# Performance work log

Measured on AMD Instinct MI355X. Metric: run time of the kernel, lower is better.

The kernel has to match this reference:

```python
import jax, jax.numpy as jnp
import numpy as np
from jax import lax

B, T, F, D, K = 64, 1000, 140, 256, 7
TAU, V_TH, EPS, ALPHA = 2.0, 1.0, 1e-5, 2.0
PAD = (K - 1) // 2

# Heaviside spike with ATan surrogate gradient (spikingjelly default, alpha=2)
@jax.custom_vjp
def spike_fn(x):
    return (x >= 0.0).astype(x.dtype)

def _spike_fwd(x):
    return spike_fn(x), x

def _spike_bwd(x, g):
    sg = (ALPHA / 2.0) / (1.0 + (jnp.pi / 2.0 * ALPHA * x) ** 2)
    return (g * sg,)

spike_fn.defvjp(_spike_fwd, _spike_bwd)

def lif(x_seq):
    """Multi-step LIF: v += (x - v)/tau, hard reset to 0 on spike. x_seq: (T,B,D)."""
    def step(v, x):
        v = v + (x - v) / TAU
        s = spike_fn(v - V_TH)
        return v * (1.0 - s), s
    _, spikes = lax.scan(step, jnp.zeros_like(x_seq[0]), x_seq)
    return spikes

def bn(x, g, b, m, v):
    # eval-mode BatchNorm1d over channel dim D (last axis of (T,B,D))
    return (x - m) * (g * lax.rsqrt(v + EPS)) + b

def setup_inputs() -> dict:
    key = jax.random.key(0)
    ks = jax.random.split(key, 4)
    s = 0.05
    return {
        "x": jax.random.normal(ks[0], (B, T, F), jnp.float32),
        "pw_w": jax.random.normal(ks[1], (D, F), jnp.float32) * s,
        "pw_b": jnp.zeros((D,), jnp.float32),
        "dw_w": jax.random.normal(ks[2], (D, 1, K), jnp.float32) * s,  # depthwise (O,I/g,K)
        "bn1_g": jnp.ones((D,), jnp.float32),
        "bn1_b": jnp.zeros((D,), jnp.float32),
        "bn1_m": jnp.zeros((D,), jnp.float32),
        "bn1_v": jnp.ones((D,), jnp.float32),
        "lin_w": jax.random.normal(ks[3], (D, D), jnp.float32) * s,
        "bn2_g": jnp.ones((D,), jnp.float32),
        "bn2_b": jnp.zeros((D,), jnp.float32),
        "bn2_m": jnp.zeros((D,), jnp.float32),
        "bn2_v": jnp.ones((D,), jnp.float32),
    }

def reference(x, pw_w, pw_b, dw_w, bn1_g, bn1_b, bn1_m, bn1_v,
              lin_w, bn2_g, bn2_b, bn2_m, bn2_v):
    # pointwise conv: (B,T,F) -> (B,D,T)
    h = jnp.einsum('btf,df->bdt', x, pw_w) + pw_b[None, :, None]
    # depthwise temporal conv, groups=D, same padding
    h = lax.conv_general_dilated(h, dw_w, window_strides=(1,),
                                 padding=[(PAD, PAD)], feature_group_count=D,
                                 dimension_numbers=('NCH', 'OIH', 'NCH'))
    h = jnp.transpose(h, (2, 0, 1))  # (T,B,D) multi-step layout
    h = lif(bn(h, bn1_g, bn1_b, bn1_m, bn1_v))
    residual = h
    h = jnp.einsum('tbd,ed->tbe', h, lin_w)
    h = lif(bn(h, bn2_g, bn2_b, bn2_m, bn2_v))
    return h + residual
```

## Files before the change

kernel.cpp:

```cpp
#include <hip/hip_runtime.h>
#include <hip/hip_bf16.h>

#define B_  64
#define T_  1000
#define F_  140
#define D_  256
#define EPS_ 1e-5f

#define CL_ 50
#define NC_ 20
#define W_  24
#define ROWS_ (CL_ + W_ + 6)

typedef __attribute__((ext_vector_type(8))) short bf16x8;
typedef __attribute__((ext_vector_type(4))) float f32x4;

static __device__ inline short f2bf(float f) {
  __hip_bfloat16 h = __float2bfloat16(f);
  return *reinterpret_cast<short*>(&h);
}
static __device__ inline float bf2f(short s) {
  unsigned int u = ((unsigned int)(unsigned short)s) << 16;
  return __uint_as_float(u);
}

__global__ __launch_bounds__(256) void k0_transpose(const float* __restrict__ lw,
                                                    float* __restrict__ lwT) {
  int i = blockIdx.x * 256 + threadIdx.x;
  int e = i >> 8, d = i & 255;
  lwT[(size_t)d * D_ + e] = lw[(size_t)e * D_ + d];
}

#define KP_ 40
__global__ __launch_bounds__(256) void k1_mfma(const float* __restrict__ x,
                                               const float* __restrict__ w,
                                               const float* __restrict__ bias,
                                               __hip_bfloat16* __restrict__ h) {
  __shared__ short smem[2 * 128 * KP_ * 2];
  short* As = smem;
  short* Bs = smem + 2 * 128 * KP_;
  const int m0 = blockIdx.x * 128;
  const int n0 = blockIdx.y * 128;
  const int tid = threadIdx.x;
  const int lane = tid & 63, wv = tid >> 6;
  const int lr = lane & 15, quad = lane >> 4;
  const int mr = (wv & 1) * 64, nc = (wv >> 1) * 64;

  const int srow = tid >> 1;
  const int sc4 = (tid & 1) * 4;

  auto stage = [&](int kc, int buf) {
#pragma unroll
    for (int c = 0; c < 4; c++) {
      int c4 = sc4 + c;
      int kg = kc + c4 * 4;
      float4 av = make_float4(0.f, 0.f, 0.f, 0.f);
      float4 bv = make_float4(0.f, 0.f, 0.f, 0.f);
      if (kg < F_) {
        av = *(const float4*)(x + (size_t)(m0 + srow) * F_ + kg);
        bv = *(const float4*)(w + (size_t)(n0 + srow) * F_ + kg);
      }
      short* ap = As + buf * 128 * KP_ + srow * KP_ + c4 * 4;
      short* bp = Bs + buf * 128 * KP_ + srow * KP_ + c4 * 4;
      ap[0] = f2bf(av.x); ap[1] = f2bf(av.y); ap[2] = f2bf(av.z); ap[3] = f2bf(av.w);
      bp[0] = f2bf(bv.x); bp[1] = f2bf(bv.y); bp[2] = f2bf(bv.z); bp[3] = f2bf(bv.w);
    }
  };

  f32x4 acc[4][4] = {};
  stage(0, 0);
  __syncthreads();
#pragma unroll
  for (int kk = 0; kk < 5; kk++) {
    const int cur = kk & 1;
    if (kk < 4) stage((kk + 1) * 32, cur ^ 1);
    const short* ab = As + cur * 128 * KP_ + quad * 8;
    const short* bb = Bs + cur * 128 * KP_ + quad * 8;
    bf16x8 a[4], b[4];
#pragma unroll
    for (int i = 0; i < 4; i++) a[i] = *(const bf16x8*)(ab + (mr + i * 16 + lr) * KP_);
#pragma unroll
    for (int j = 0; j < 4; j++) b[j] = *(const bf16x8*)(bb + (nc + j * 16 + lr) * KP_);
#pragma unroll
    for (int i = 0; i < 4; i++)
#pragma unroll
      for (int j = 0; j < 4; j++)
        acc[i][j] = __builtin_amdgcn_mfma_f32_16x16x32_bf16(a[i], b[j], acc[i][j], 0, 0, 0);
    __syncthreads();
  }

  short* Cs = smem;
#pragma unroll
  for (int j = 0; j < 4; j++) {
    const int n = nc + j * 16 + lr;
    const float badd = bias[n0 + n];
#pragma unroll
    for (int i = 0; i < 4; i++) {
      const int mrow = mr + i * 16 + quad * 4;
#pragma unroll
      for (int r = 0; r < 4; r++)
        Cs[(mrow + r) * 136 + n] = f2bf(acc[i][j][r] + badd);
    }
  }
  __syncthreads();
  const int row = tid >> 1, half = tid & 1;
  const int m = m0 + row;
  const int bb2 = m / T_;
  const int t = m - bb2 * T_;
  __hip_bfloat16* dst = h + ((size_t)t * B_ + bb2) * D_ + n0 + half * 64;
  const short* src = Cs + row * 136 + half * 64;
#pragma unroll
  for (int c = 0; c < 4; c++)
    *(int4*)(dst + c * 8) = *(const int4*)(src + c * 8);
}

__global__ __launch_bounds__(256) void k2_dw_lif(const __hip_bfloat16* __restrict__ h,
                                                 const float* __restrict__ dww,
                                                 const float* __restrict__ g1,
                                                 const float* __restrict__ b1,
                                                 const float* __restrict__ m1,
                                                 const float* __restrict__ v1,
                                                 unsigned long long* __restrict__ bits) {
  __shared__ short hs[ROWS_ * D_];
  const int b = blockIdx.x;
  const int t0 = blockIdx.y * CL_;
  const int tstart = (t0 >= W_) ? t0 - W_ : 0;
  const int nwarm = t0 - tstart;
  const int nrows = nwarm + CL_ + 6;
  const int tid = threadIdx.x;

  {
    const int c8 = (tid & 31) * 8;
    for (int r = tid >> 5; r < nrows; r += 8) {
      const int t = tstart - 3 + r;
      bf16x8 val = {0, 0, 0, 0, 0, 0, 0, 0};
      if (t >= 0 && t < T_)
        val = *(const bf16x8*)((const short*)h + ((size_t)t * B_ + b) * D_ + c8);
      *(bf16x8*)(hs + r * D_ + c8) = val;
    }
  }
  __syncthreads();

  const int d = tid;
  float w[7];
#pragma unroll
  for (int k = 0; k < 7; k++) w[k] = dww[d * 7 + k];
  const float sc = g1[d] * rsqrtf(v1[d] + EPS_);
  const float shf = b1[d] - m1[d] * sc;

  float win0 = bf2f(hs[0 * D_ + d]);
  float win1 = bf2f(hs[1 * D_ + d]);
  float win2 = bf2f(hs[2 * D_ + d]);
  float win3 = bf2f(hs[3 * D_ + d]);
  float win4 = bf2f(hs[4 * D_ + d]);
  float win5 = bf2f(hs[5 * D_ + d]);
  float v = 0.f;
  int s = 0;
  for (; s < nwarm; s++) {
    float tap6 = bf2f(hs[(s + 6) * D_ + d]);
    float conv = win0 * w[0] + win1 * w[1] + win2 * w[2] + win3 * w[3] +
                 win4 * w[4] + win5 * w[5] + tap6 * w[6];
    float u = conv * sc + shf;
    v = 0.5f * (v + u);
    v = (v >= 1.0f) ? 0.f : v;
    win0 = win1; win1 = win2; win2 = win3; win3 = win4; win4 = win5; win5 = tap6;
  }
  unsigned long long* bp = bits + ((size_t)b * T_ + t0) * 4 + (tid >> 6);
  const bool lane0 = (tid & 63) == 0;
#pragma unroll 5
  for (int i = 0; i < CL_; i++, s++) {
    float tap6 = bf2f(hs[(s + 6) * D_ + d]);
    float conv = win0 * w[0] + win1 * w[1] + win2 * w[2] + win3 * w[3] +
                 win4 * w[4] + win5 * w[5] + tap6 * w[6];
    float u = conv * sc + shf;
    v = 0.5f * (v + u);
    bool sp = (v >= 1.0f);
    unsigned long long mask = __ballot(sp);
    if (lane0) bp[(size_t)i * 4] = mask;
    v = sp ? 0.f : v;
    win0 = win1; win1 = win2; win2 = win3; win3 = win4; win4 = win5; win5 = tap6;
  }
}

__global__ __launch_bounds__(256) void k3_lin_lif(const unsigned long long* __restrict__ bits,
                                                  const float* __restrict__ lwT,
                                                  const float* __restrict__ g2,
                                                  const float* __restrict__ b2,
                                                  const float* __restrict__ m2,
                                                  const float* __restrict__ v2,
                                                  float* __restrict__ out) {
  __shared__ unsigned long long sb[(CL_ + W_) * 4];
  const int b = blockIdx.x;
  const int t0 = blockIdx.y * CL_;
  const int tstart = (t0 >= W_) ? t0 - W_ : 0;
  const int nwarm = t0 - tstart;
  const int nsteps = nwarm + CL_;
  const int e = threadIdx.x;
  const unsigned long long* gbp = bits + ((size_t)b * T_ + tstart) * 4;
  for (int i = e; i < nsteps * 4; i += 256) sb[i] = gbp[i];
  __syncthreads();

  const float sc = g2[e] * rsqrtf(v2[e] + EPS_);
  const float shf = b2[e] - m2[e] * sc;
  const int eq = e >> 6, eb = e & 63;
  float v = 0.f;
  int s = 0;
  for (; s < nwarm; s++) {
    unsigned long long w0 = sb[s * 4 + 0], w1 = sb[s * 4 + 1];
    unsigned long long w2 = sb[s * 4 + 2], w3 = sb[s * 4 + 3];
    float acc = 0.f;
    if (w0 | w1 | w2 | w3) {
      unsigned long long mm;
      mm = w0; while (mm) { int l = __builtin_ctzll(mm); mm &= mm - 1; acc += lwT[(size_t)(l) * D_ + e]; }
      mm = w1; while (mm) { int l = __builtin_ctzll(mm); mm &= mm - 1; acc += lwT[(size_t)(64 + l) * D_ + e]; }
      mm = w2; while (mm) { int l = __builtin_ctzll(mm); mm &= mm - 1; acc += lwT[(size_t)(128 + l) * D_ + e]; }
      mm = w3; while (mm) { int l = __builtin_ctzll(mm); mm &= mm - 1; acc += lwT[(size_t)(192 + l) * D_ + e]; }
    }
    float u = acc * sc + shf;
    v = 0.5f * (v + u);
    v = (v >= 1.0f) ? 0.f : v;
  }
  float* op = out + ((size_t)t0 * B_ + b) * D_ + e;
  const size_t ts = (size_t)B_ * D_;
#pragma unroll 5
  for (int i = 0; i < CL_; i++, s++) {
    unsigned long long w0 = sb[s * 4 + 0], w1 = sb[s * 4 + 1];
    unsigned long long w2 = sb[s * 4 + 2], w3 = sb[s * 4 + 3];
    float acc = 0.f;
    if (w0 | w1 | w2 | w3) {
      unsigned long long mm;
      mm = w0; while (mm) { int l = __builtin_ctzll(mm); mm &= mm - 1; acc += lwT[(size_t)(l) * D_ + e]; }
      mm = w1; while (mm) { int l = __builtin_ctzll(mm); mm &= mm - 1; acc += lwT[(size_t)(64 + l) * D_ + e]; }
      mm = w2; while (mm) { int l = __builtin_ctzll(mm); mm &= mm - 1; acc += lwT[(size_t)(128 + l) * D_ + e]; }
      mm = w3; while (mm) { int l = __builtin_ctzll(mm); mm &= mm - 1; acc += lwT[(size_t)(192 + l) * D_ + e]; }
    }
    float u = acc * sc + shf;
    v = 0.5f * (v + u);
    bool sp = (v >= 1.0f);
    unsigned long long myw = sb[s * 4 + eq];
    float s1 = (float)((myw >> eb) & 1ull);
    op[(size_t)i * ts] = (sp ? 1.0f : 0.0f) + s1;
    v = sp ? 0.f : v;
  }
}

extern "C" void kernel_launch(void* const* d_in, const int* in_sizes, int n_in,
                              void* d_out, int out_size, void* d_ws, size_t ws_size,
                              hipStream_t stream) {
  const float* x    = (const float*)d_in[0];
  const float* pw_w = (const float*)d_in[1];
  const float* pw_b = (const float*)d_in[2];
  const float* dw_w = (const float*)d_in[3];
  const float* g1   = (const float*)d_in[4];
  const float* b1   = (const float*)d_in[5];
  const float* m1   = (const float*)d_in[6];
  const float* v1   = (const float*)d_in[7];
  const float* lw   = (const float*)d_in[8];
  const float* g2   = (const float*)d_in[9];
  const float* b2   = (const float*)d_in[10];
  const float* m2   = (const float*)d_in[11];
  const float* v2   = (const float*)d_in[12];
  float* out = (float*)d_out;

  char* ws = (char*)d_ws;
  __hip_bfloat16* h = (__hip_bfloat16*)ws;
  unsigned long long* bits = (unsigned long long*)(ws + 32768000);
  float* lwT = (float*)(ws + 32768000 + 2048000);

  k0_transpose<<<(D_ * D_) / 256, 256, 0, stream>>>(lw, lwT);
  dim3 g_gemm((B_ * T_) / 128, D_ / 128);
  k1_mfma<<<g_gemm, 256, 0, stream>>>(x, pw_w, pw_b, h);
  dim3 g_scan(B_, NC_);
  k2_dw_lif<<<g_scan, 256, 0, stream>>>(h, dw_w, g1, b1, m1, v1, bits);
  k3_lin_lif<<<g_scan, 256, 0, stream>>>(bits, lwT, g2, b2, m2, v2, out);
}
```

Before: 177.7 us.

## Fuse pointwise GEMM with depthwise conv and first LIF scan

Merges the MFMA pointwise projection and the depthwise-conv/LIF kernel into one kernel. Each block computes a 128-row by 256-channel GEMM tile for one batch and a time chunk (95 new steps plus overlap), then runs the conv and scan straight from shared memory. This removes the bf16 h intermediate round trip through global memory and one launch. The pointwise weights are converted to padded bf16 once in the prep kernel. In exchange, the grid drops to 64x11 blocks, each with 128 accumulator registers per thread, and GEMM rows in the warmup overlap are recomputed across chunks.

```diff
diff --git a/kernel.cpp b/kernel.cpp
--- a/kernel.cpp
+++ b/kernel.cpp
@@ -10,9 +10,12 @@
 #define CL_ 50
 #define NC_ 20
 #define W_  24
-#define ROWS_ (CL_ + W_ + 6)
+
+#define CW_  95
+#define NCH_ 11
 
 typedef __attribute__((ext_vector_type(8))) short bf16x8;
+typedef __attribute__((ext_vector_type(4))) short bf16x4;
 typedef __attribute__((ext_vector_type(4))) float f32x4;
 
 static __device__ inline short f2bf(float f) {
@@ -24,119 +27,107 @@
   return __uint_as_float(u);
 }
 
-__global__ __launch_bounds__(256) void k0_transpose(const float* __restrict__ lw,
-                                                    float* __restrict__ lwT) {
+__global__ __launch_bounds__(256) void k0_prep(const float* __restrict__ lw,
+                                               float* __restrict__ lwT,
+                                               const float* __restrict__ pw,
+                                               short* __restrict__ wbf) {
   int i = blockIdx.x * 256 + threadIdx.x;
-  int e = i >> 8, d = i & 255;
-  lwT[(size_t)d * D_ + e] = lw[(size_t)e * D_ + d];
-}
-
-#define KP_ 40
-__global__ __launch_bounds__(256) void k1_mfma(const float* __restrict__ x,
-                                               const float* __restrict__ w,
-                                               const float* __restrict__ bias,
-                                               __hip_bfloat16* __restrict__ h) {
-  __shared__ short smem[2 * 128 * KP_ * 2];
+  if (i < 65536) {
+    int e = i >> 8, d = i & 255;
+    lwT[(size_t)d * D_ + e] = lw[(size_t)e * D_ + d];
+  } else if (i < 65536 + 256 * 160) {
+    int j = i - 65536;
+    int n = j / 160, k = j - n * 160;
+    wbf[j] = (k < F_) ? f2bf(pw[(size_t)n * F_ + k]) : (short)0;
+  }
+}
+
+__global__ __launch_bounds__(256, 2) void k12_fused(const float* __restrict__ x,
+                                                    const short* __restrict__ wbf,
+                                                    const float* __restrict__ bias,
+                                                    const float* __restrict__ dww,
+                                                    const float* __restrict__ g1,
+                                                    const float* __restrict__ b1,
+                                                    const float* __restrict__ m1,
+                                                    const float* __restrict__ v1,
+                                                    unsigned long long* __restrict__ bits) {
+  __shared__ short smem[32768];
   short* As = smem;
-  short* Bs = smem + 2 * 128 * KP_;
-  const int m0 = blockIdx.x * 128;
-  const int n0 = blockIdx.y * 128;
+  short* Bs = smem + 10240;
+  const int b = blockIdx.x;
+  const int c = blockIdx.y;
+  const int a = CW_ * c;
   const int tid = threadIdx.x;
   const int lane = tid & 63, wv = tid >> 6;
   const int lr = lane & 15, quad = lane >> 4;
-  const int mr = (wv & 1) * 64, nc = (wv >> 1) * 64;
+  const int mr = (wv & 1) * 64;
+  const int nc0 = (wv >> 1) * 128;
 
   const int srow = tid >> 1;
   const int sc4 = (tid & 1) * 4;
+  const bool arow_ok = (a + srow) < T_;
+  const float* xrow = x + ((size_t)b * T_ + a + srow) * F_;
+  const short* wsrc0 = wbf + (size_t)tid * 160;
 
   auto stage = [&](int kc, int buf) {
-#pragma unroll
-    for (int c = 0; c < 4; c++) {
-      int c4 = sc4 + c;
+    short* abase = As + buf * (128 * 40) + srow * 40;
+#pragma unroll
+    for (int s = 0; s < 4; s++) {
+      int c4 = sc4 + s;
       int kg = kc + c4 * 4;
       float4 av = make_float4(0.f, 0.f, 0.f, 0.f);
-      float4 bv = make_float4(0.f, 0.f, 0.f, 0.f);
-      if (kg < F_) {
-        av = *(const float4*)(x + (size_t)(m0 + srow) * F_ + kg);
-        bv = *(const float4*)(w + (size_t)(n0 + srow) * F_ + kg);
-      }
-      short* ap = As + buf * 128 * KP_ + srow * KP_ + c4 * 4;
-      short* bp = Bs + buf * 128 * KP_ + srow * KP_ + c4 * 4;
-      ap[0] = f2bf(av.x); ap[1] = f2bf(av.y); ap[2] = f2bf(av.z); ap[3] = f2bf(av.w);
-      bp[0] = f2bf(bv.x); bp[1] = f2bf(bv.y); bp[2] = f2bf(bv.z); bp[3] = f2bf(bv.w);
-    }
+      if (arow_ok && kg < F_) av = *(const float4*)(xrow + kg);
+      bf16x4 pk = {f2bf(av.x), f2bf(av.y), f2bf(av.z), f2bf(av.w)};
+      *(bf16x4*)(abase + c4 * 4) = pk;
+    }
+    short* bbase = Bs + buf * (256 * 40) + tid * 40;
+    const short* wsrc = wsrc0 + kc;
+#pragma unroll
+    for (int s = 0; s < 4; s++)
+      *(bf16x8*)(bbase + s * 8) = *(const bf16x8*)(wsrc + s * 8);
   };
 
-  f32x4 acc[4][4] = {};
+  f32x4 acc[4][8] = {};
   stage(0, 0);
   __syncthreads();
 #pragma unroll
   for (int kk = 0; kk < 5; kk++) {
     const int cur = kk & 1;
     if (kk < 4) stage((kk + 1) * 32, cur ^ 1);
-    const short* ab = As + cur * 128 * KP_ + quad * 8;
-    const short* bb = Bs + cur * 128 * KP_ + quad * 8;
-    bf16x8 a[4], b[4];
-#pragma unroll
-    for (int i = 0; i < 4; i++) a[i] = *(const bf16x8*)(ab + (mr + i * 16 + lr) * KP_);
-#pragma unroll
-    for (int j = 0; j < 4; j++) b[j] = *(const bf16x8*)(bb + (nc + j * 16 + lr) * KP_);
+    const short* ap = As + cur * (128 * 40) + quad * 8;
+    const short* bp = Bs + cur * (256 * 40) + quad * 8;
+    bf16x8 af[4], bfr[8];
+#pragma unroll
+    for (int i = 0; i < 4; i++) af[i] = *(const bf16x8*)(ap + (mr + i * 16 + lr) * 40);
+#pragma unroll
+    for (int j = 0; j < 8; j++) bfr[j] = *(const bf16x8*)(bp + (nc0 + j * 16 + lr) * 40);
 #pragma unroll
     for (int i = 0; i < 4; i++)
 #pragma unroll
-      for (int j = 0; j < 4; j++)
-        acc[i][j] = __builtin_amdgcn_mfma_f32_16x16x32_bf16(a[i], b[j], acc[i][j], 0, 0, 0);
+      for (int j = 0; j < 8; j++)
+        acc[i][j] = __builtin_amdgcn_mfma_f32_16x16x32_bf16(af[i], bfr[j], acc[i][j], 0, 0, 0);
     __syncthreads();
   }
 
-  short* Cs = smem;
-#pragma unroll
-  for (int j = 0; j < 4; j++) {
-    const int n = nc + j * 16 + lr;
-    const float badd = bias[n0 + n];
+  short* hbuf = smem;
+  if (c == 0) {
+    hbuf[0 * D_ + tid] = 0; hbuf[1 * D_ + tid] = 0; hbuf[2 * D_ + tid] = 0;
+  }
+#pragma unroll
+  for (int j = 0; j < 8; j++) {
+    const int n = nc0 + j * 16 + lr;
+    const float badd = bias[n];
 #pragma unroll
     for (int i = 0; i < 4; i++) {
-      const int mrow = mr + i * 16 + quad * 4;
-#pragma unroll
-      for (int r = 0; r < 4; r++)
-        Cs[(mrow + r) * 136 + n] = f2bf(acc[i][j][r] + badd);
-    }
-  }
-  __syncthreads();
-  const int row = tid >> 1, half = tid & 1;
-  const int m = m0 + row;
-  const int bb2 = m / T_;
-  const int t = m - bb2 * T_;
-  __hip_bfloat16* dst = h + ((size_t)t * B_ + bb2) * D_ + n0 + half * 64;
-  const short* src = Cs + row * 136 + half * 64;
-#pragma unroll
-  for (int c = 0; c < 4; c++)
-    *(int4*)(dst + c * 8) = *(const int4*)(src + c * 8);
-}
-
-__global__ __launch_bounds__(256) void k2_dw_lif(const __hip_bfloat16* __restrict__ h,
-                                                 const float* __restrict__ dww,
-                                                 const float* __restrict__ g1,
-                                                 const float* __restrict__ b1,
-                                                 const float* __restrict__ m1,
-                                                 const float* __restrict__ v1,
-                                                 unsigned long long* __restrict__ bits) {
-  __shared__ short hs[ROWS_ * D_];
-  const int b = blockIdx.x;
-  const int t0 = blockIdx.y * CL_;
-  const int tstart = (t0 >= W_) ? t0 - W_ : 0;
-  const int nwarm = t0 - tstart;
-  const int nrows = nwarm + CL_ + 6;
-  const int tid = threadIdx.x;
-
-  {
-    const int c8 = (tid & 31) * 8;
-    for (int r = tid >> 5; r < nrows; r += 8) {
-      const int t = tstart - 3 + r;
-      bf16x8 val = {0, 0, 0, 0, 0, 0, 0, 0};
-      if (t >= 0 && t < T_)
-        val = *(const bf16x8*)((const short*)h + ((size_t)t * B_ + b) * D_ + c8);
-      *(bf16x8*)(hs + r * D_ + c8) = val;
+      const int m = mr + i * 16 + quad * 4;
+#pragma unroll
+      for (int r = 0; r < 4; r++) {
+        const int mm = m + r;
+        if (mm < 125) {
+          short val = ((a + mm) < T_) ? f2bf(acc[i][j][r] + badd) : (short)0;
+          hbuf[(mm + 3) * D_ + n] = val;
+        }
+      }
     }
   }
   __syncthreads();
@@ -148,16 +139,22 @@
   const float sc = g1[d] * rsqrtf(v1[d] + EPS_);
   const float shf = b1[d] - m1[d] * sc;
 
-  float win0 = bf2f(hs[0 * D_ + d]);
-  float win1 = bf2f(hs[1 * D_ + d]);
-  float win2 = bf2f(hs[2 * D_ + d]);
-  float win3 = bf2f(hs[3 * D_ + d]);
-  float win4 = bf2f(hs[4 * D_ + d]);
-  float win5 = bf2f(hs[5 * D_ + d]);
+  const int lt0 = (c == 0) ? 0 : 3;
+  const int nwarm = (c == 0) ? 0 : W_;
+  const int tw0 = a + ((c == 0) ? 0 : 27);
+  int nwrite = (c == 0) ? 122 : CW_;
+  if (nwrite > T_ - tw0) nwrite = T_ - tw0;
+
+  float win0 = bf2f(hbuf[(lt0 + 0) * D_ + d]);
+  float win1 = bf2f(hbuf[(lt0 + 1) * D_ + d]);
+  float win2 = bf2f(hbuf[(lt0 + 2) * D_ + d]);
+  float win3 = bf2f(hbuf[(lt0 + 3) * D_ + d]);
+  float win4 = bf2f(hbuf[(lt0 + 4) * D_ + d]);
+  float win5 = bf2f(hbuf[(lt0 + 5) * D_ + d]);
   float v = 0.f;
   int s = 0;
   for (; s < nwarm; s++) {
-    float tap6 = bf2f(hs[(s + 6) * D_ + d]);
+    float tap6 = bf2f(hbuf[(lt0 + s + 6) * D_ + d]);
     float conv = win0 * w[0] + win1 * w[1] + win2 * w[2] + win3 * w[3] +
                  win4 * w[4] + win5 * w[5] + tap6 * w[6];
     float u = conv * sc + shf;
@@ -165,18 +162,17 @@
     v = (v >= 1.0f) ? 0.f : v;
     win0 = win1; win1 = win2; win2 = win3; win3 = win4; win4 = win5; win5 = tap6;
   }
-  unsigned long long* bp = bits + ((size_t)b * T_ + t0) * 4 + (tid >> 6);
-  const bool lane0 = (tid & 63) == 0;
-#pragma unroll 5
-  for (int i = 0; i < CL_; i++, s++) {
-    float tap6 = bf2f(hs[(s + 6) * D_ + d]);
+  unsigned long long* bp2 = bits + ((size_t)b * T_ + tw0) * 4 + wv;
+  const bool lane0 = (lane == 0);
+  for (int i2 = 0; i2 < nwrite; i2++, s++) {
+    float tap6 = bf2f(hbuf[(lt0 + s + 6) * D_ + d]);
     float conv = win0 * w[0] + win1 * w[1] + win2 * w[2] + win3 * w[3] +
                  win4 * w[4] + win5 * w[5] + tap6 * w[6];
     float u = conv * sc + shf;
     v = 0.5f * (v + u);
     bool sp = (v >= 1.0f);
     unsigned long long mask = __ballot(sp);
-    if (lane0) bp[(size_t)i * 4] = mask;
+    if (lane0) bp2[(size_t)i2 * 4] = mask;
     v = sp ? 0.f : v;
     win0 = win1; win1 = win2; win2 = win3; win3 = win4; win4 = win5; win5 = tap6;
   }
@@ -263,14 +259,13 @@
   float* out = (float*)d_out;
 
   char* ws = (char*)d_ws;
-  __hip_bfloat16* h = (__hip_bfloat16*)ws;
-  unsigned long long* bits = (unsigned long long*)(ws + 32768000);
-  float* lwT = (float*)(ws + 32768000 + 2048000);
-
-  k0_transpose<<<(D_ * D_) / 256, 256, 0, stream>>>(lw, lwT);
-  dim3 g_gemm((B_ * T_) / 128, D_ / 128);
-  k1_mfma<<<g_gemm, 256, 0, stream>>>(x, pw_w, pw_b, h);
-  dim3 g_scan(B_, NC_);
-  k2_dw_lif<<<g_scan, 256, 0, stream>>>(h, dw_w, g1, b1, m1, v1, bits);
-  k3_lin_lif<<<g_scan, 256, 0, stream>>>(bits, lwT, g2, b2, m2, v2, out);
-}
+  unsigned long long* bits = (unsigned long long*)ws;
+  float* lwT = (float*)(ws + 2048000);
+  short* wbf = (short*)(ws + 2048000 + 262144);
+
+  k0_prep<<<(65536 + 256 * 160 + 255) / 256, 256, 0, stream>>>(lw, lwT, pw_w, wbf);
+  dim3 g_k12(B_, NCH_);
+  k12_fused<<<g_k12, 256, 0, stream>>>(x, wbf, pw_b, dw_w, g1, b1, m1, v1, bits);
+  dim3 g_k3(B_, NC_);
+  k3_lin_lif<<<g_k3, 256, 0, stream>>>(bits, lwT, g2, b2, m2, v2, out);
+}
```

Result: faster. 169.2 us (-4.8%).
